# Kernel tuning notes

Measured on AMD Instinct MI355X. Metric: run time of the kernel, lower is better.

Reference implementation:

```python
import jax, jax.numpy as jnp
import numpy as np

B, T, D = 32, 1024, 1024
H = 512        # LSTM units per direction
L = 3          # num_layers


def _run_lstm(x, mask, W, U, b):
    """Masked unidirectional LSTM, Keras gate order (i, f, c, o).
    x: [B,T,D], mask: [B,T] bool (True = valid). Masked steps carry state
    and repeat the previous output, matching Keras masking semantics."""
    z_all = jnp.einsum('btd,dk->tbk', x, W) + b          # [T,B,4H]
    m_all = jnp.transpose(mask, (1, 0))                   # [T,B]

    def step(carry, inp):
        h, c = carry
        z_t, m_t = inp
        z = z_t + h @ U                                   # [B,4H]
        i, f, g, o = jnp.split(z, 4, axis=-1)
        i = jax.nn.sigmoid(i)
        f = jax.nn.sigmoid(f)
        g = jnp.tanh(g)
        o = jax.nn.sigmoid(o)
        c_new = f * c + i * g
        h_new = o * jnp.tanh(c_new)
        m = m_t[:, None]
        h = jnp.where(m, h_new, h)
        c = jnp.where(m, c_new, c)
        return (h, c), h

    h0 = jnp.zeros((x.shape[0], U.shape[0]), x.dtype)
    (_, _), hs = jax.lax.scan(step, (h0, h0), (z_all, m_all))
    return jnp.transpose(hs, (1, 0, 2))                   # [B,T,H]


def _bilstm(x, mask, Wf, Uf, bf, Wb, Ub, bb):
    fwd = _run_lstm(x, mask, Wf, Uf, bf)
    bwd = _run_lstm(x[:, ::-1], mask[:, ::-1], Wb, Ub, bb)[:, ::-1]
    return jnp.concatenate([fwd, bwd], axis=-1)           # [B,T,2H]


def setup_inputs() -> dict:
    key = jax.random.key(0)
    ks = jax.random.split(key, 16)
    s = 0.05
    inp = {
        'x': jax.random.normal(ks[0], (B, T, D), jnp.float32),
        'x_mask': jax.random.randint(ks[1], (B, T), 0, 2, jnp.int32),
        # stacked BiLSTM params (all layers share shapes since 2H == D)
        'Wf': jax.random.normal(ks[2], (L, D, 4 * H), jnp.float32) * s,
        'Uf': jax.random.normal(ks[3], (L, H, 4 * H), jnp.float32) * s,
        'bf': jax.random.normal(ks[4], (L, 4 * H), jnp.float32) * s,
        'Wb': jax.random.normal(ks[5], (L, D, 4 * H), jnp.float32) * s,
        'Ub': jax.random.normal(ks[6], (L, H, 4 * H), jnp.float32) * s,
        'bb': jax.random.normal(ks[7], (L, 4 * H), jnp.float32) * s,
        # task heads
        'Wp': jax.random.normal(ks[8], (2 * H, 2), jnp.float32) * s,
        'bp': jnp.zeros((2,), jnp.float32),
        'Wbu': jax.random.normal(ks[9], (2 * H, 2), jnp.float32) * s,
        'bbu': jnp.zeros((2,), jnp.float32),
        'Wss3': jax.random.normal(ks[10], (2 * H, 3), jnp.float32) * s,
        'bss3': jnp.zeros((3,), jnp.float32),
        'Wss8': jax.random.normal(ks[11], (2 * H, 8), jnp.float32) * s,
        'bss8': jnp.zeros((8,), jnp.float32),
        'training': 0,
    }
    return inp


def reference(x, x_mask, Wf, Uf, bf, Wb, Ub, bb, Wp, bp, Wbu, bbu,
              Wss3, bss3, Wss8, bss8, training):
    # mask = not(x_mask == 1): True = valid position
    mask = x_mask != 1
    for l in range(L):
        x = _bilstm(x, mask, Wf[l], Uf[l], bf[l], Wb[l], Ub[l], bb[l])
    x = jax.nn.relu(x)
    # dropout is identity at inference (training == 0)
    ppi = jax.nn.softmax(x @ Wp + bp, axis=-1)
    buried = x @ Wbu + bbu
    ss3 = x @ Wss3 + bss3
    ss8 = x @ Wss8 + bss8
    return (ppi, buried, ss3, ss8)
```

## Files before the change

kernel.cpp:

```cpp
#include <hip/hip_runtime.h>
#include <hip/hip_bf16.h>
#include <math.h>


#define B_ 32
#define T_ 1024
#define H_ 512
#define NG 2048

typedef __attribute__((ext_vector_type(8))) short bf16x8;
typedef __attribute__((ext_vector_type(4))) float f32x4;
typedef unsigned int u32;
typedef unsigned short u16;

__device__ inline u16 f2bf(float f) {
    u32 u = __float_as_uint(f);
    return (u16)((u + 0x7fffu + ((u >> 16) & 1u)) >> 16);
}
__device__ inline float bf2f(u16 v) { return __uint_as_float(((u32)v) << 16); }
__device__ inline void gload16(const void* g, void* l) {
    __builtin_amdgcn_global_load_lds(
        (const __attribute__((address_space(1))) u32*)g,
        (__attribute__((address_space(3))) u32*)l, 16, 0, 0);
}
__device__ inline float fsig(float x) { return 1.0f / (1.0f + __expf(-x)); }
__device__ inline float ftanh(float x) { return 1.0f - 2.0f / (__expf(2.0f * x) + 1.0f); }

__global__ void zero_mem(float* __restrict__ s, int n) {
    int i = blockIdx.x * 256 + threadIdx.x;
    if (i < n) s[i] = 0.0f;
}

__global__ __launch_bounds__(256) void conv_bf16(const float* __restrict__ src,
                                                 u16* __restrict__ dst) {
    int i = blockIdx.x * 256 + threadIdx.x;
    float4 v = *(const float4*)&src[(size_t)i * 4];
    ushort4 o = { f2bf(v.x), f2bf(v.y), f2bf(v.z), f2bf(v.w) };
    *(ushort4*)&dst[(size_t)i * 4] = o;
}

__global__ __launch_bounds__(256) void transpose_w(const float* __restrict__ Wf,
                                                   const float* __restrict__ Wb,
                                                   u16* __restrict__ wt) {
    int mat = blockIdx.z;
    const float* W = ((mat & 1) ? Wb : Wf) + (size_t)(mat >> 1) * 1024 * NG;
    u16* dst = wt + (size_t)mat * NG * 1024;
    __shared__ float tile[64][65];
    int n0 = blockIdx.x * 64, k0 = blockIdx.y * 64;
    int t = threadIdx.x;
#pragma unroll
    for (int i = 0; i < 16; ++i) {
        int idx = t + i * 256;
        int kk = idx >> 6, nn = idx & 63;
        tile[kk][nn] = W[(size_t)(k0 + kk) * NG + n0 + nn];
    }
    __syncthreads();
#pragma unroll
    for (int i = 0; i < 16; ++i) {
        int idx = t + i * 256;
        int nn = idx >> 6, kk = idx & 63;
        dst[(size_t)(n0 + nn) * 1024 + k0 + kk] = f2bf(tile[kk][nn]);
    }
}

__global__ __launch_bounds__(256) void pack_u(const float* __restrict__ Uf,
                                              const float* __restrict__ Ub,
                                              u16* __restrict__ upk) {
    int mat = blockIdx.y;
    const float* U = ((mat & 1) ? Ub : Uf) + (size_t)(mat >> 1) * H_ * NG;
    u16* dst = upk + (size_t)mat * 1048576;
    int f = blockIdx.x * 256 + threadIdx.x;
    int lane = f & 63, ks = (f >> 6) & 15, c2 = (f >> 10) & 1;
    int cp = (f >> 11) & 3, wg = f >> 13;
    int col = cp * H_ + wg * 32 + c2 * 16 + (lane & 15);
    int krow = ks * 32 + (lane >> 4) * 8;
    u16 o[8];
#pragma unroll
    for (int j = 0; j < 8; ++j) o[j] = f2bf(U[(size_t)(krow + j) * NG + col]);
    *(uint4*)(dst + (size_t)f * 8) = *(uint4*)o;
}

__global__ __launch_bounds__(256) void gemm_mfma(
    const u16* __restrict__ A, const u16* __restrict__ Bt,
    const float* __restrict__ bias, u16* __restrict__ Zb,
    int t0, int lgC) {
    __shared__ __align__(16) u16 sA[128 * 32];
    __shared__ __align__(16) u16 sB[128 * 32];
    const int tid = threadIdx.x;
    const int m0 = blockIdx.y * 128, n0 = blockIdx.x * 128;
    const int Cmask = (1 << lgC) - 1;

    const int chunk0 = tid, chunk1 = tid + 256;
    const int r0 = chunk0 >> 2, kp0 = (chunk0 & 3) * 8;
    const int r1 = chunk1 >> 2, kp1 = (chunk1 & 3) * 8;
    const int gm0 = m0 + r0, gm1 = m0 + r1;
    const size_t arow0 = ((size_t)(gm0 >> lgC) * T_ + t0 + (gm0 & Cmask)) * 1024;
    const size_t arow1 = ((size_t)(gm1 >> lgC) * T_ + t0 + (gm1 & Cmask)) * 1024;
    const size_t brow0 = (size_t)(n0 + r0) * 1024;
    const size_t brow1 = (size_t)(n0 + r1) * 1024;

    const int lane = tid & 63, wave = tid >> 6;
    const int wr = (wave >> 1) * 64, wc = (wave & 1) * 64;
    const int fr = lane & 15, fk = (lane >> 4) * 8;

    f32x4 acc[4][4] = {};
    for (int kc = 0; kc < 1024; kc += 32) {
        gload16(A + arow0 + kc + kp0, &sA[chunk0 * 8]);
        gload16(A + arow1 + kc + kp1, &sA[chunk1 * 8]);
        gload16(Bt + brow0 + kc + kp0, &sB[chunk0 * 8]);
        gload16(Bt + brow1 + kc + kp1, &sB[chunk1 * 8]);
        __syncthreads();
        bf16x8 af[4], bfr[4];
#pragma unroll
        for (int i = 0; i < 4; ++i)
            af[i] = *(const bf16x8*)&sA[(wr + i * 16 + fr) * 32 + fk];
#pragma unroll
        for (int j = 0; j < 4; ++j)
            bfr[j] = *(const bf16x8*)&sB[(wc + j * 16 + fr) * 32 + fk];
#pragma unroll
        for (int i = 0; i < 4; ++i)
#pragma unroll
            for (int j = 0; j < 4; ++j)
                acc[i][j] = __builtin_amdgcn_mfma_f32_16x16x32_bf16(
                    af[i], bfr[j], acc[i][j], 0, 0, 0);
        __syncthreads();
    }
    float bv[4];
    int un[4], gn[4];
#pragma unroll
    for (int j = 0; j < 4; ++j) {
        int n = n0 + wc + j * 16 + fr;
        bv[j] = bias[n];
        un[j] = n & 511; gn[j] = n >> 9;
    }
#pragma unroll
    for (int i = 0; i < 4; ++i) {
        int mb = m0 + wr + i * 16 + (lane >> 4) * 4;
#pragma unroll
        for (int j = 0; j < 4; ++j) {
#pragma unroll
            for (int r = 0; r < 4; ++r)
                Zb[(size_t)(mb + r) * 2048 + un[j] * 4 + gn[j]] =
                    f2bf(acc[i][j][r] + bv[j]);
        }
    }
}

__global__ __launch_bounds__(512, 1) void lstm_chunk(
    const u16* __restrict__ zf, const u16* __restrict__ zb,
    const u16* __restrict__ upk,
    const int* __restrict__ xmask,
    u32* __restrict__ hbuf32,
    float* __restrict__ cst, float* __restrict__ hst,
    u32* __restrict__ flags,
    u16* __restrict__ hseq,
    int t0f, int t0b, int C, int sbase) {
    const int bx = blockIdx.x, dir = bx >> 4, wgs = bx & 15, u0 = wgs * 32;
    const u16* z = dir ? zb : zf;
    const u16* up = upk + dir * 1048576;
    u32* hb32 = hbuf32 + dir * 16384;
    u32* myflag = flags + (dir * 16 + wgs) * 32;
    const u32* fbase = flags + dir * 512;
    const int tid = threadIdx.x;
    const int wave = tid >> 6, lane = tid & 63;
    const int cp = wave & 3, bt = wave >> 2, fr = lane & 15, fq = lane >> 4;
    const int row = bt * 16 + fr;
    const int swz = (row & 7) << 4;

    __shared__ __align__(16) u16 sh[16384];
    __shared__ float sacc[32 * 132];

    bf16x8 uf0[16], uf1[16];
#pragma unroll
    for (int ks = 0; ks < 16; ++ks) {
        size_t base0 = (((size_t)(wgs * 4 + cp) * 2) * 16 + ks) * 512 + lane * 8;
        uf0[ks] = *(const bf16x8*)(up + base0);
        uf1[ks] = *(const bf16x8*)(up + base0 + 16 * 512);
    }

    const int b0p = tid >> 5, ul = tid & 31, b1p = b0p + 16, ug = u0 + ul;
    const int sidx = (dir * 16 + wgs) * 1024 + tid * 2;
    float c0r = cst[sidx], c1r = cst[sidx + 1];
    float h0r = hst[sidx], h1r = hst[sidx + 1];
    const size_t hs0 = (size_t)b0p * T_ * 1024 + dir * 512 + ug;
    const size_t hs1 = (size_t)b1p * T_ * 1024 + dir * 512 + ug;

    {
        u32 tmp[16];
#pragma unroll
        for (int k = 0; k < 16; ++k)
            tmp[k] = __hip_atomic_load(hb32 + k * 512 + tid, __ATOMIC_RELAXED,
                                       __HIP_MEMORY_SCOPE_AGENT);
#pragma unroll
        for (int k = 0; k < 16; ++k) {
            int idx = k * 512 + tid;
            int sb = (idx * 4) ^ (((idx >> 8) & 7) << 4);
            *(u32*)((char*)sh + sb) = tmp[k];
        }
    }
    ushort4 za0, za1; int mc0, mc1;
    {
        int tc = dir ? (C - 1) : 0;
        int t = dir ? (t0b + C - 1) : t0f;
        za0 = *(const ushort4*)(z + ((size_t)(b0p * C + tc)) * 2048 + ug * 4);
        za1 = *(const ushort4*)(z + ((size_t)(b1p * C + tc)) * 2048 + ug * 4);
        mc0 = xmask[b0p * T_ + t]; mc1 = xmask[b1p * T_ + t];
    }
    __syncthreads();

    u16 hb0s = 0, hb1s = 0;
    for (int st = 0; st < C; ++st) {
        const int t = dir ? (t0b + C - 1 - st) : (t0f + st);
        u32* nx32 = hb32 + (((st & 1) ^ 1) ? 8192 : 0);

        f32x4 acc0 = {0, 0, 0, 0}, acc1 = {0, 0, 0, 0};
#pragma unroll
        for (int ks = 0; ks < 16; ++ks) {
            int abyte = (row * 1024 + ks * 64 + fq * 16) ^ swz;
            bf16x8 a = *(const bf16x8*)((const char*)sh + abyte);
            acc0 = __builtin_amdgcn_mfma_f32_16x16x32_bf16(a, uf0[ks], acc0, 0, 0, 0);
            acc1 = __builtin_amdgcn_mfma_f32_16x16x32_bf16(a, uf1[ks], acc1, 0, 0, 0);
        }
#pragma unroll
        for (int j = 0; j < 4; ++j) {
            int b = bt * 16 + fq * 4 + j;
            sacc[b * 132 + cp * 32 + fr] = acc0[j];
            sacc[b * 132 + cp * 32 + 16 + fr] = acc1[j];
        }
        __syncthreads();
        {
            const float* s0 = sacc + b0p * 132;
            const float* s1 = sacc + b1p * 132;
            float i0 = fsig(bf2f(za0.x) + s0[ul]);
            float f0 = fsig(bf2f(za0.y) + s0[32 + ul]);
            float g0 = ftanh(bf2f(za0.z) + s0[64 + ul]);
            float o0 = fsig(bf2f(za0.w) + s0[96 + ul]);
            if (mc0 != 1) { c0r = f0 * c0r + i0 * g0; h0r = o0 * ftanh(c0r); }
            float i1 = fsig(bf2f(za1.x) + s1[ul]);
            float f1 = fsig(bf2f(za1.y) + s1[32 + ul]);
            float g1 = ftanh(bf2f(za1.z) + s1[64 + ul]);
            float o1 = fsig(bf2f(za1.w) + s1[96 + ul]);
            if (mc1 != 1) { c1r = f1 * c1r + i1 * g1; h1r = o1 * ftanh(c1r); }
            hb0s = f2bf(h0r); hb1s = f2bf(h1r);
            u32 nb0 = __shfl_xor((u32)hb0s, 1, 64);
            u32 nb1 = __shfl_xor((u32)hb1s, 1, 64);
            if ((ul & 1) == 0) {
                u32 pk0 = (u32)hb0s | (nb0 << 16);
                u32 pk1 = (u32)hb1s | (nb1 << 16);
                __hip_atomic_store(nx32 + b0p * 256 + (ug >> 1), pk0,
                                   __ATOMIC_RELAXED, __HIP_MEMORY_SCOPE_AGENT);
                __hip_atomic_store(nx32 + b1p * 256 + (ug >> 1), pk1,
                                   __ATOMIC_RELAXED, __HIP_MEMORY_SCOPE_AGENT);
            }
        }
        asm volatile("s_waitcnt vmcnt(0)" ::: "memory");
        __syncthreads();
        const u32 tgt = (u32)(sbase + st + 1);
        if (tid == 0)
            __hip_atomic_store(myflag, tgt, __ATOMIC_RELAXED,
                               __HIP_MEMORY_SCOPE_AGENT);
        ushort4 zn0, zn1; int mn0, mn1;
        {
            int stn = (st + 1 < C) ? st + 1 : st;
            int tcn = dir ? (C - 1 - stn) : stn;
            int tn = dir ? (t0b + tcn) : (t0f + tcn);
            zn0 = *(const ushort4*)(z + ((size_t)(b0p * C + tcn)) * 2048 + ug * 4);
            zn1 = *(const ushort4*)(z + ((size_t)(b1p * C + tcn)) * 2048 + ug * 4);
            mn0 = xmask[b0p * T_ + tn]; mn1 = xmask[b1p * T_ + tn];
        }
        if (wave == 0) {
            const u32* fp = fbase + (lane & 15) * 32;
            u32 v;
            do {
                v = __hip_atomic_load(fp, __ATOMIC_RELAXED,
                                      __HIP_MEMORY_SCOPE_AGENT);
            } while (!__all(v >= tgt));
        }
        __syncthreads();
        if (st + 1 < C) {
            const u32* src = hb32 + (((st + 1) & 1) ? 8192 : 0);
            u32 tmp[16];
#pragma unroll
            for (int k = 0; k < 16; ++k)
                tmp[k] = __hip_atomic_load(src + k * 512 + tid, __ATOMIC_RELAXED,
                                           __HIP_MEMORY_SCOPE_AGENT);
#pragma unroll
            for (int k = 0; k < 16; ++k) {
                int idx = k * 512 + tid;
                int sb = (idx * 4) ^ (((idx >> 8) & 7) << 4);
                *(u32*)((char*)sh + sb) = tmp[k];
            }
        }
        hseq[hs0 + (size_t)t * 1024] = hb0s;
        hseq[hs1 + (size_t)t * 1024] = hb1s;
        za0 = zn0; za1 = zn1; mc0 = mn0; mc1 = mn1;
        __syncthreads();
    }
    cst[sidx] = c0r; cst[sidx + 1] = c1r;
    hst[sidx] = h0r; hst[sidx + 1] = h1r;
}

__global__ __launch_bounds__(256) void heads_kernel(
    const u16* __restrict__ xin,
    const float* __restrict__ Wp, const float* __restrict__ bp,
    const float* __restrict__ Wbu, const float* __restrict__ bbu,
    const float* __restrict__ Wss3, const float* __restrict__ bss3,
    const float* __restrict__ Wss8, const float* __restrict__ bss8,
    float* __restrict__ out) {
    const int r = blockIdx.x * 4 + (threadIdx.x >> 6);
    const int lane = threadIdx.x & 63;
    const u16* xr = xin + (size_t)r * 1024 + lane * 16;
    uint4 q0 = *(const uint4*)xr;
    uint4 q1 = *(const uint4*)(xr + 8);
    float xv[16];
    u32 qs[8] = { q0.x, q0.y, q0.z, q0.w, q1.x, q1.y, q1.z, q1.w };
#pragma unroll
    for (int i = 0; i < 8; ++i) {
        xv[i * 2]     = fmaxf(__uint_as_float((qs[i] & 0xffffu) << 16), 0.0f);
        xv[i * 2 + 1] = fmaxf(__uint_as_float(qs[i] & 0xffff0000u), 0.0f);
    }
    float acc[15] = {};
    const int k0 = lane * 16;
#pragma unroll
    for (int kk = 0; kk < 16; kk++) {
        float xk = xv[kk];
        int k = k0 + kk;
        acc[0] += xk * Wp[k * 2];      acc[1] += xk * Wp[k * 2 + 1];
        acc[2] += xk * Wbu[k * 2];     acc[3] += xk * Wbu[k * 2 + 1];
        acc[4] += xk * Wss3[k * 3];    acc[5] += xk * Wss3[k * 3 + 1];
        acc[6] += xk * Wss3[k * 3 + 2];
#pragma unroll
        for (int o = 0; o < 8; o++) acc[7 + o] += xk * Wss8[k * 8 + o];
    }
#pragma unroll
    for (int o = 0; o < 15; o++) {
#pragma unroll
        for (int off = 32; off; off >>= 1) acc[o] += __shfl_xor(acc[o], off, 64);
    }
    if (lane == 0) {
        float a0 = acc[0] + bp[0], a1 = acc[1] + bp[1];
        float mx = fmaxf(a0, a1);
        float e0 = expf(a0 - mx), e1 = expf(a1 - mx);
        float ssum = e0 + e1;
        out[(size_t)r * 2] = e0 / ssum;
        out[(size_t)r * 2 + 1] = e1 / ssum;
        float* ob = out + 65536;
        ob[r * 2] = acc[2] + bbu[0]; ob[r * 2 + 1] = acc[3] + bbu[1];
        float* o3 = out + 131072;
        o3[r * 3 + 0] = acc[4] + bss3[0];
        o3[r * 3 + 1] = acc[5] + bss3[1];
        o3[r * 3 + 2] = acc[6] + bss3[2];
        float* o8 = out + 229376;
#pragma unroll
        for (int o = 0; o < 8; o++) o8[r * 8 + o] = acc[7 + o] + bss8[o];
    }
}

extern "C" void kernel_launch(void* const* d_in, const int* in_sizes, int n_in,
                              void* d_out, int out_size, void* d_ws, size_t ws_size,
                              hipStream_t stream) {
    const float* x = (const float*)d_in[0];
    const int* xmask = (const int*)d_in[1];
    const float* Wf = (const float*)d_in[2];
    const float* Uf = (const float*)d_in[3];
    const float* bfp = (const float*)d_in[4];
    const float* Wb = (const float*)d_in[5];
    const float* Ub = (const float*)d_in[6];
    const float* bbp = (const float*)d_in[7];
    const float* Wp = (const float*)d_in[8];
    const float* bp = (const float*)d_in[9];
    const float* Wbu = (const float*)d_in[10];
    const float* bbu = (const float*)d_in[11];
    const float* Wss3 = (const float*)d_in[12];
    const float* bss3 = (const float*)d_in[13];
    const float* Wss8 = (const float*)d_in[14];
    const float* bss8 = (const float*)d_in[15];

    char* wsb = (char*)d_ws;
    u16* actA = (u16*)wsb;
    u16* actB = (u16*)(wsb + (64ull << 20));
    u16* wt   = (u16*)(wsb + (128ull << 20));
    u16* upk  = (u16*)(wsb + (152ull << 20));
    char* stb = wsb + (164ull << 20);
    u32* hbuf32 = (u32*)stb;
    float* cst = (float*)(stb + 131072);
    float* hst = (float*)(stb + 262144);
    u32* flags = (u32*)(stb + 393216);
    const int stateFloats = (393216 + 4096) / 4;

    size_t fixedB = 165ull << 20;
    int C = 1024;
    while (C > 128 && fixedB + 262144ull * C > ws_size) C >>= 1;
    int lgC = 31 - __builtin_clz((unsigned)C);
    u16* zf = (u16*)(wsb + fixedB);
    u16* zb = zf + (size_t)B_ * C * 2048;

    conv_bf16<<<dim3(8388608 / 256), 256, 0, stream>>>(x, actA);
    transpose_w<<<dim3(32, 16, 6), 256, 0, stream>>>(Wf, Wb, wt);
    pack_u<<<dim3(512, 6), 256, 0, stream>>>(Uf, Ub, upk);

    const u16* cur = actA;
    for (int l = 0; l < 3; l++) {
        u16* dst = (l & 1) ? actA : actB;
        zero_mem<<<dim3((stateFloats + 255) / 256), 256, 0, stream>>>(
            (float*)stb, stateFloats);
        u16* wtf = wt + (size_t)(l * 2 + 0) * NG * 1024;
        u16* wtb = wt + (size_t)(l * 2 + 1) * NG * 1024;
        const u16* upkl = upk + (size_t)l * 2 * 1048576;
        const float* bfl = bfp + l * NG;
        const float* bbl = bbp + l * NG;
        for (int c0 = 0; c0 < T_; c0 += C) {
            int t0f = c0;
            int t0b = T_ - c0 - C;
            dim3 ggrid(NG / 128, (B_ * C) / 128);
            gemm_mfma<<<ggrid, 256, 0, stream>>>(cur, wtf, bfl, zf, t0f, lgC);
            gemm_mfma<<<ggrid, 256, 0, stream>>>(cur, wtb, bbl, zb, t0b, lgC);

            const u16* a_zf = zf; const u16* a_zb = zb;
            const u16* a_up = upkl; const int* a_xm = xmask;
            u32* a_hb = hbuf32; float* a_cs = cst; float* a_hs = hst;
            u32* a_fl = flags; u16* a_hseq = dst;
            int a_t0f = t0f, a_t0b = t0b, a_C = C, a_sb = c0;
            void* kargs[] = { &a_zf, &a_zb, &a_up, &a_xm, &a_hb, &a_cs, &a_hs,
                              &a_fl, &a_hseq, &a_t0f, &a_t0b, &a_C, &a_sb };
            hipLaunchCooperativeKernel((void*)lstm_chunk, dim3(32), dim3(512),
                                       kargs, 0, stream);
        }
        cur = dst;
    }
    heads_kernel<<<dim3(B_ * T_ / 4), 256, 0, stream>>>(
        cur, Wp, bp, Wbu, bbu, Wss3, bss3, Wss8, bss8, (float*)d_out);
}
```

Before: 12.11 ms.

## Replace per-step flag barrier with step-tagged 64-bit hidden-state words

The cross-workgroup handoff of the recurrent hidden state now packs a step tag into the upper 32 bits of each 64-bit word. Consumers spin on the data words themselves until every tag matches the expected step, so the vmcnt drain, the extra __syncthreads and the per-workgroup flag store and poll are no longer needed. This removes a full publish-then-poll round trip from the serial critical path of every timestep. In exchange the exchange buffers are twice as large, every thread polls 16 words instead of one wave polling 16 flags, and correctness depends on each 64-bit store being observed atomically.

Result: slower. 22.12 ms (+82.7%).

```diff
diff --git a/kernel.cpp b/kernel.cpp
--- a/kernel.cpp
+++ b/kernel.cpp
@@ -11,6 +11,7 @@
 typedef __attribute__((ext_vector_type(8))) short bf16x8;
 typedef __attribute__((ext_vector_type(4))) float f32x4;
 typedef unsigned int u32;
+typedef unsigned long long u64;
 typedef unsigned short u16;
 
 __device__ inline u16 f2bf(float f) {
@@ -150,17 +151,14 @@
     const u16* __restrict__ zf, const u16* __restrict__ zb,
     const u16* __restrict__ upk,
     const int* __restrict__ xmask,
-    u32* __restrict__ hbuf32,
+    u64* __restrict__ hbuf64,
     float* __restrict__ cst, float* __restrict__ hst,
-    u32* __restrict__ flags,
     u16* __restrict__ hseq,
     int t0f, int t0b, int C, int sbase) {
     const int bx = blockIdx.x, dir = bx >> 4, wgs = bx & 15, u0 = wgs * 32;
     const u16* z = dir ? zb : zf;
     const u16* up = upk + dir * 1048576;
-    u32* hb32 = hbuf32 + dir * 16384;
-    u32* myflag = flags + (dir * 16 + wgs) * 32;
-    const u32* fbase = flags + dir * 512;
+    u64* hb64 = hbuf64 + dir * 16384;
     const int tid = threadIdx.x;
     const int wave = tid >> 6, lane = tid & 63;
     const int cp = wave & 3, bt = wave >> 2, fr = lane & 15, fq = lane >> 4;
@@ -186,16 +184,26 @@
     const size_t hs1 = (size_t)b1p * T_ * 1024 + dir * 512 + ug;
 
     {
-        u32 tmp[16];
-#pragma unroll
-        for (int k = 0; k < 16; ++k)
-            tmp[k] = __hip_atomic_load(hb32 + k * 512 + tid, __ATOMIC_RELAXED,
-                                       __HIP_MEMORY_SCOPE_AGENT);
+        const u64* src = hb64 + ((sbase & 1) ? 8192 : 0);
+        const u32 tg0 = (u32)sbase;
+        u32 pend = 0xffffu;
+        u64 got[16];
+        do {
+#pragma unroll
+            for (int k = 0; k < 16; ++k) {
+                if (pend & (1u << k)) {
+                    u64 v = __hip_atomic_load(src + k * 512 + tid,
+                                              __ATOMIC_RELAXED,
+                                              __HIP_MEMORY_SCOPE_AGENT);
+                    if ((u32)(v >> 32) == tg0) { got[k] = v; pend &= ~(1u << k); }
+                }
+            }
+        } while (pend);
 #pragma unroll
         for (int k = 0; k < 16; ++k) {
             int idx = k * 512 + tid;
             int sb = (idx * 4) ^ (((idx >> 8) & 7) << 4);
-            *(u32*)((char*)sh + sb) = tmp[k];
+            *(u32*)((char*)sh + sb) = (u32)got[k];
         }
     }
     ushort4 za0, za1; int mc0, mc1;
@@ -208,10 +216,10 @@
     }
     __syncthreads();
 
-    u16 hb0s = 0, hb1s = 0;
     for (int st = 0; st < C; ++st) {
         const int t = dir ? (t0b + C - 1 - st) : (t0f + st);
-        u32* nx32 = hb32 + (((st & 1) ^ 1) ? 8192 : 0);
+        const u32 tgt = (u32)(sbase + st + 1);
+        u64* nx64 = hb64 + ((tgt & 1) ? 8192 : 0);
 
         f32x4 acc0 = {0, 0, 0, 0}, acc1 = {0, 0, 0, 0};
 #pragma unroll
@@ -241,59 +249,50 @@
             float g1 = ftanh(bf2f(za1.z) + s1[64 + ul]);
             float o1 = fsig(bf2f(za1.w) + s1[96 + ul]);
             if (mc1 != 1) { c1r = f1 * c1r + i1 * g1; h1r = o1 * ftanh(c1r); }
-            hb0s = f2bf(h0r); hb1s = f2bf(h1r);
+            u16 hb0s = f2bf(h0r), hb1s = f2bf(h1r);
             u32 nb0 = __shfl_xor((u32)hb0s, 1, 64);
             u32 nb1 = __shfl_xor((u32)hb1s, 1, 64);
             if ((ul & 1) == 0) {
-                u32 pk0 = (u32)hb0s | (nb0 << 16);
-                u32 pk1 = (u32)hb1s | (nb1 << 16);
-                __hip_atomic_store(nx32 + b0p * 256 + (ug >> 1), pk0,
+                u64 w0 = ((u64)tgt << 32) | (u32)hb0s | (nb0 << 16);
+                u64 w1 = ((u64)tgt << 32) | (u32)hb1s | (nb1 << 16);
+                __hip_atomic_store(nx64 + b0p * 256 + (ug >> 1), w0,
                                    __ATOMIC_RELAXED, __HIP_MEMORY_SCOPE_AGENT);
-                __hip_atomic_store(nx32 + b1p * 256 + (ug >> 1), pk1,
+                __hip_atomic_store(nx64 + b1p * 256 + (ug >> 1), w1,
                                    __ATOMIC_RELAXED, __HIP_MEMORY_SCOPE_AGENT);
             }
-        }
-        asm volatile("s_waitcnt vmcnt(0)" ::: "memory");
-        __syncthreads();
-        const u32 tgt = (u32)(sbase + st + 1);
-        if (tid == 0)
-            __hip_atomic_store(myflag, tgt, __ATOMIC_RELAXED,
-                               __HIP_MEMORY_SCOPE_AGENT);
-        ushort4 zn0, zn1; int mn0, mn1;
+            hseq[hs0 + (size_t)t * 1024] = hb0s;
+            hseq[hs1 + (size_t)t * 1024] = hb1s;
+        }
         {
             int stn = (st + 1 < C) ? st + 1 : st;
             int tcn = dir ? (C - 1 - stn) : stn;
             int tn = dir ? (t0b + tcn) : (t0f + tcn);
-            zn0 = *(const ushort4*)(z + ((size_t)(b0p * C + tcn)) * 2048 + ug * 4);
-            zn1 = *(const ushort4*)(z + ((size_t)(b1p * C + tcn)) * 2048 + ug * 4);
-            mn0 = xmask[b0p * T_ + tn]; mn1 = xmask[b1p * T_ + tn];
-        }
-        if (wave == 0) {
-            const u32* fp = fbase + (lane & 15) * 32;
-            u32 v;
+            za0 = *(const ushort4*)(z + ((size_t)(b0p * C + tcn)) * 2048 + ug * 4);
+            za1 = *(const ushort4*)(z + ((size_t)(b1p * C + tcn)) * 2048 + ug * 4);
+            mc0 = xmask[b0p * T_ + tn]; mc1 = xmask[b1p * T_ + tn];
+        }
+        if (st + 1 < C) {
+            const u64* src = nx64;
+            u32 pend = 0xffffu;
+            u64 got[16];
             do {
-                v = __hip_atomic_load(fp, __ATOMIC_RELAXED,
-                                      __HIP_MEMORY_SCOPE_AGENT);
-            } while (!__all(v >= tgt));
-        }
-        __syncthreads();
-        if (st + 1 < C) {
-            const u32* src = hb32 + (((st + 1) & 1) ? 8192 : 0);
-            u32 tmp[16];
-#pragma unroll
-            for (int k = 0; k < 16; ++k)
-                tmp[k] = __hip_atomic_load(src + k * 512 + tid, __ATOMIC_RELAXED,
-                                           __HIP_MEMORY_SCOPE_AGENT);
+#pragma unroll
+                for (int k = 0; k < 16; ++k) {
+                    if (pend & (1u << k)) {
+                        u64 v = __hip_atomic_load(src + k * 512 + tid,
+                                                  __ATOMIC_RELAXED,
+                                                  __HIP_MEMORY_SCOPE_AGENT);
+                        if ((u32)(v >> 32) == tgt) { got[k] = v; pend &= ~(1u << k); }
+                    }
+                }
+            } while (pend);
 #pragma unroll
             for (int k = 0; k < 16; ++k) {
                 int idx = k * 512 + tid;
                 int sb = (idx * 4) ^ (((idx >> 8) & 7) << 4);
-                *(u32*)((char*)sh + sb) = tmp[k];
+                *(u32*)((char*)sh + sb) = (u32)got[k];
             }
         }
-        hseq[hs0 + (size_t)t * 1024] = hb0s;
-        hseq[hs1 + (size_t)t * 1024] = hb1s;
-        za0 = zn0; za1 = zn1; mc0 = mn0; mc1 = mn1;
         __syncthreads();
     }
     cst[sidx] = c0r; cst[sidx + 1] = c1r;
@@ -382,11 +381,10 @@
     u16* wt   = (u16*)(wsb + (128ull << 20));
     u16* upk  = (u16*)(wsb + (152ull << 20));
     char* stb = wsb + (164ull << 20);
-    u32* hbuf32 = (u32*)stb;
-    float* cst = (float*)(stb + 131072);
-    float* hst = (float*)(stb + 262144);
-    u32* flags = (u32*)(stb + 393216);
-    const int stateFloats = (393216 + 4096) / 4;
+    u64* hbuf64 = (u64*)stb;
+    float* cst = (float*)(stb + 262144);
+    float* hst = (float*)(stb + 393216);
+    const int stateFloats = 524288 / 4;
 
     size_t fixedB = 165ull << 20;
     int C = 1024;
@@ -418,11 +416,11 @@
 
             const u16* a_zf = zf; const u16* a_zb = zb;
             const u16* a_up = upkl; const int* a_xm = xmask;
-            u32* a_hb = hbuf32; float* a_cs = cst; float* a_hs = hst;
-            u32* a_fl = flags; u16* a_hseq = dst;
+            u64* a_hb = hbuf64; float* a_cs = cst; float* a_hs = hst;
+            u16* a_hseq = dst;
             int a_t0f = t0f, a_t0b = t0b, a_C = C, a_sb = c0;
             void* kargs[] = { &a_zf, &a_zb, &a_up, &a_xm, &a_hb, &a_cs, &a_hs,
-                              &a_fl, &a_hseq, &a_t0f, &a_t0b, &a_C, &a_sb };
+                              &a_hseq, &a_t0f, &a_t0b, &a_C, &a_sb };
             hipLaunchCooperativeKernel((void*)lstm_chunk, dim3(32), dim3(512),
                                        kargs, 0, stream);
         }
```
